# Optimization experiments

Measured on AMD Instinct MI355X. Metric: run time of the kernel, lower is better.

## Reference

```python
import jax, jax.numpy as jnp
import numpy as np

B, N, C = 32, 577, 768
H = 12
DH = C // H  # 64
SCALE = DH ** -0.5


def setup_inputs() -> dict:
    key = jax.random.key(0)
    ks = jax.random.split(key, 5)
    x = jax.random.normal(ks[0], (B, N, C), dtype=jnp.float32)
    # Linear params (torch convention: y = x @ W.T + b)
    qkv_w = jax.random.normal(ks[1], (3 * C, C), dtype=jnp.float32) * (C ** -0.5)
    qkv_b = jnp.zeros((3 * C,), dtype=jnp.float32)
    proj_w = jax.random.normal(ks[2], (C, C), dtype=jnp.float32) * (C ** -0.5)
    proj_b = jnp.zeros((C,), dtype=jnp.float32)
    return {"x": x, "qkv_w": qkv_w, "qkv_b": qkv_b, "proj_w": proj_w, "proj_b": proj_b}


def reference(x, qkv_w, qkv_b, proj_w, proj_b):
    b, n, c = x.shape
    qkv = x @ qkv_w.T + qkv_b                       # [B, N, 3C]
    qkv = qkv.reshape(b, n, 3, H, DH).transpose(2, 0, 3, 1, 4)  # [3, B, H, N, DH]
    q, k, v = qkv[0], qkv[1], qkv[2]
    q = q * SCALE
    attn = jnp.einsum('bhnd,bhmd->bhnm', q, k)      # [B, H, N, N]
    # sigmoid -> inverse-sigmoid straight-through rewrite (forward equals logit(sigmoid(attn)))
    sig = jax.nn.sigmoid(attn)
    inv_sig = jnp.log(sig / (1.0 - sig))
    attn_st = attn + jax.lax.stop_gradient(inv_sig - attn)
    p = jax.nn.softmax(attn_st, axis=-1)
    out = jnp.einsum('bhnm,bhmd->bhnd', p, v)       # [B, H, N, DH]
    out = out.transpose(0, 2, 1, 3).reshape(b, n, c)
    return out @ proj_w.T + proj_b
```

## Files before the change

### kernel.cpp

```cpp
#include <hip/hip_runtime.h>

typedef __bf16 bf16;
typedef __attribute__((ext_vector_type(4))) __bf16 bf16x4;
typedef __attribute__((ext_vector_type(8))) __bf16 bf16x8;
typedef __attribute__((ext_vector_type(4))) float f32x4;

#define MFMA_BF16(A_, B_, C_) __builtin_amdgcn_mfma_f32_16x16x32_bf16(A_, B_, C_, 0, 0, 0)

#define BB    32
#define SEQ   577
#define CH    768
#define NH    12
#define DHD   64
#define MROWS (BB * SEQ)
#define NQKV  2304
#define SEQP  584
#define QSCALE 0.1803368801111204f

__device__ __forceinline__ void async_ld16(const bf16* g, bf16* l) {
  __builtin_amdgcn_global_load_lds(
      (const __attribute__((address_space(1))) void*)g,
      (__attribute__((address_space(3))) void*)l, 16, 0, 0);
}

__global__ __launch_bounds__(256) void cvt_bf16(const float* __restrict__ src,
                                                bf16* __restrict__ dst, int n) {
  int idx = (blockIdx.x * 256 + threadIdx.x) * 4;
  if (idx >= n) return;
  float4 v = *(const float4*)(src + idx);
  bf16x4 o = {(bf16)v.x, (bf16)v.y, (bf16)v.z, (bf16)v.w};
  *(bf16x4*)(dst + idx) = o;
}

template <int EPI>
__global__ __launch_bounds__(256, 5)
void gemm_bt(const bf16* __restrict__ A, const bf16* __restrict__ W,
             const float* __restrict__ bias,
             bf16* __restrict__ qrm, bf16* __restrict__ krm, bf16* __restrict__ vt,
             float* __restrict__ out) {
  __shared__ bf16 As[2][128 * 32];
  __shared__ bf16 Bs[2][128 * 32];
  const int tid = threadIdx.x, lane = tid & 63, wid = tid >> 6;
  const int quad = lane >> 4, r15 = lane & 15;

  const int nbx = (int)gridDim.x;
  const int nwg = nbx * (int)gridDim.y;
  int bid = (int)blockIdx.y * nbx + (int)blockIdx.x;
  int q8 = nwg >> 3, r8 = nwg & 7;
  int xcd = bid & 7, sub = bid >> 3;
  int wg = (xcd < r8 ? xcd * (q8 + 1) : r8 * (q8 + 1) + (xcd - r8) * q8) + sub;
  const int m0 = (wg / nbx) * 128, n0 = (wg % nbx) * 128;
  const int waveM = wid & 1, waveN = wid >> 1;

  const bf16* aSrc[2];
  const bf16* bSrc[2];
  for (int c = 0; c < 2; ++c) {
    int q = wid * 128 + c * 64 + lane;
    int row = q >> 2;
    int sw = (row ^ (row >> 2)) & 3;
    int kc = (q & 3) ^ sw;
    aSrc[c] = A + (size_t)(m0 + row) * CH + kc * 8;
    bSrc[c] = W + (size_t)(n0 + row) * CH + kc * 8;
  }

  f32x4 acc[4][4];
#pragma unroll
  for (int i = 0; i < 4; ++i)
#pragma unroll
    for (int j = 0; j < 4; ++j) acc[i][j] = (f32x4){0.f, 0.f, 0.f, 0.f};

#define GSTAGE(K0, BUF)                                                   \
  {                                                                       \
    _Pragma("unroll") for (int c = 0; c < 2; ++c) {                       \
      async_ld16(aSrc[c] + (K0), &As[BUF][(wid * 128 + c * 64) * 8]);     \
      async_ld16(bSrc[c] + (K0), &Bs[BUF][(wid * 128 + c * 64) * 8]);     \
    }                                                                     \
  }

#define GCOMPUTE(BUF)                                                     \
  {                                                                       \
    bf16x8 af[4], bfr[4];                                                 \
    _Pragma("unroll") for (int s = 0; s < 4; ++s) {                       \
      int rowA = waveM * 64 + s * 16 + r15;                               \
      int ca = quad ^ ((rowA ^ (rowA >> 2)) & 3);                         \
      af[s] = *(const bf16x8*)(&As[BUF][rowA * 32 + ca * 8]);             \
      int rowB = waveN * 64 + s * 16 + r15;                               \
      int cb = quad ^ ((rowB ^ (rowB >> 2)) & 3);                         \
      bfr[s] = *(const bf16x8*)(&Bs[BUF][rowB * 32 + cb * 8]);            \
    }                                                                     \
    _Pragma("unroll") for (int sm = 0; sm < 4; ++sm)                      \
      _Pragma("unroll") for (int sn = 0; sn < 4; ++sn)                    \
        acc[sm][sn] = MFMA_BF16(af[sm], bfr[sn], acc[sm][sn]);            \
  }

  GSTAGE(0, 0);
  for (int k0 = 0; k0 < CH; k0 += 64) {
    __syncthreads();
    GSTAGE(k0 + 32, 1);
    GCOMPUTE(0);
    __syncthreads();
    if (k0 + 64 < CH) GSTAGE(k0 + 64, 0);
    GCOMPUTE(1);
  }

  if (EPI == 0) {
    int t = (n0 >= 1536) ? 2 : (n0 >= 768 ? 1 : 0);
#pragma unroll
    for (int sn = 0; sn < 4; ++sn) {
      int gn = n0 + waveN * 64 + sn * 16 + r15;
      float bv = bias[gn];
      int col = gn - t * CH;
      int h = col >> 6, d = col & 63;
#pragma unroll
      for (int sm = 0; sm < 4; ++sm) {
        int gmBase = m0 + waveM * 64 + sm * 16 + quad * 4;
#pragma unroll
        for (int r = 0; r < 4; ++r) {
          int gm = gmBase + r;
          if (gm < MROWS) {
            float v = acc[sm][sn][r] + bv;
            if (t == 0) {
              qrm[(size_t)gm * CH + col] = (bf16)(v * QSCALE);
            } else if (t == 1) {
              krm[(size_t)gm * CH + col] = (bf16)v;
            } else {
              int b_ = gm / SEQ;
              int n_ = gm - b_ * SEQ;
              vt[((size_t)(b_ * NH + h) * DHD + d) * SEQP + n_] = (bf16)v;
            }
          }
        }
      }
    }
  } else {
#pragma unroll
    for (int sn = 0; sn < 4; ++sn) {
      int gn = n0 + waveN * 64 + sn * 16 + r15;
      float bv = bias[gn];
#pragma unroll
      for (int sm = 0; sm < 4; ++sm) {
        int gmBase = m0 + waveM * 64 + sm * 16 + quad * 4;
#pragma unroll
        for (int r = 0; r < 4; ++r) {
          int gm = gmBase + r;
          if (gm < MROWS) out[(size_t)gm * CH + gn] = acc[sm][sn][r] + bv;
        }
      }
    }
  }
}

__global__ __launch_bounds__(256, 6)
void attn_kernel(const bf16* __restrict__ qrm, const bf16* __restrict__ krm,
                 const bf16* __restrict__ vt, bf16* __restrict__ ob) {
  __shared__ bf16 Ks[64 * 72];
  __shared__ bf16 Vt[64 * 72];
  const int tid = threadIdx.x, lane = tid & 63, wid = tid >> 6;
  const int quad = lane >> 4, r15 = lane & 15;
  const int qt = blockIdx.x, bh = blockIdx.y;
  const int b_ = bh / NH, h = bh - b_ * NH;
  const bf16* vtb = vt + (size_t)bh * DHD * SEQP;

  int qrow = qt * 64 + wid * 16 + r15;
  if (qrow > SEQ - 1) qrow = SEQ - 1;
  const bf16* qp = qrm + (size_t)(b_ * SEQ + qrow) * CH + h * DHD + quad * 8;
  bf16x8 qf0 = *(const bf16x8*)qp;
  bf16x8 qf1 = *(const bf16x8*)(qp + 32);

  f32x4 oacc[4];
#pragma unroll
  for (int i = 0; i < 4; ++i) oacc[i] = (f32x4){0.f, 0.f, 0.f, 0.f};
  float lrow[4] = {0.f, 0.f, 0.f, 0.f};

  for (int j0 = 0; j0 < SEQ; j0 += 64) {
    __syncthreads();
#pragma unroll
    for (int c = 0; c < 2; ++c) {
      int sid = c * 256 + tid;
      int row = sid >> 3, cc = sid & 7;
      int jr = j0 + row;
      if (jr > SEQ - 1) jr = SEQ - 1;
      *(bf16x8*)(Ks + row * 72 + cc * 8) =
          *(const bf16x8*)(krm + (size_t)(b_ * SEQ + jr) * CH + h * DHD + cc * 8);
      int jst = j0 + cc * 8;
      if (jst > SEQ - 1) jst = SEQ - 1;
      *(bf16x8*)(Vt + row * 72 + cc * 8) = *(const bf16x8*)(vtb + (size_t)row * SEQP + jst);
    }
    __syncthreads();

    f32x4 s[4];
#pragma unroll
    for (int sj = 0; sj < 4; ++sj) {
      bf16x8 kf0 = *(const bf16x8*)(Ks + (sj * 16 + r15) * 72 + quad * 8);
      bf16x8 kf1 = *(const bf16x8*)(Ks + (sj * 16 + r15) * 72 + 32 + quad * 8);
      f32x4 z = (f32x4){0.f, 0.f, 0.f, 0.f};
      s[sj] = MFMA_BF16(qf0, kf0, z);
      s[sj] = MFMA_BF16(qf1, kf1, s[sj]);
    }
#pragma unroll
    for (int sj = 0; sj < 4; ++sj)
      if (j0 + sj * 16 + r15 > SEQ - 1) s[sj] = (f32x4){-1e30f, -1e30f, -1e30f, -1e30f};

#pragma unroll
    for (int sj = 0; sj < 4; ++sj)
#pragma unroll
      for (int r = 0; r < 4; ++r) {
        float e = __builtin_amdgcn_exp2f(s[sj][r]);
        s[sj][r] = e;
        lrow[r] += e;
      }

    __syncthreads();
    bf16* Pw = Ks + wid * (16 * 72);
#pragma unroll
    for (int sj = 0; sj < 4; ++sj)
#pragma unroll
      for (int r = 0; r < 4; ++r)
        Pw[(quad * 4 + r) * 72 + sj * 16 + r15] = (bf16)s[sj][r];
    asm volatile("s_waitcnt lgkmcnt(0)" ::: "memory");

#pragma unroll
    for (int kc = 0; kc < 2; ++kc) {
      bf16x8 pf = *(const bf16x8*)(Pw + r15 * 72 + kc * 32 + quad * 8);
#pragma unroll
      for (int sd = 0; sd < 4; ++sd) {
        bf16x8 vf = *(const bf16x8*)(Vt + (sd * 16 + r15) * 72 + kc * 32 + quad * 8);
        oacc[sd] = MFMA_BF16(pf, vf, oacc[sd]);
      }
    }
  }

#pragma unroll
  for (int r = 0; r < 4; ++r) {
    float rs = lrow[r];
    rs += __shfl_xor(rs, 1);
    rs += __shfl_xor(rs, 2);
    rs += __shfl_xor(rs, 4);
    rs += __shfl_xor(rs, 8);
    lrow[r] = rs;
  }

#pragma unroll
  for (int r = 0; r < 4; ++r) {
    int orow = qt * 64 + wid * 16 + quad * 4 + r;
    if (orow < SEQ) {
      float inv = 1.0f / lrow[r];
      size_t rowoff = ((size_t)(b_ * SEQ + orow)) * CH + h * DHD;
#pragma unroll
      for (int sd = 0; sd < 4; ++sd)
        ob[rowoff + sd * 16 + r15] = (bf16)(oacc[sd][r] * inv);
    }
  }
}

extern "C" void kernel_launch(void* const* d_in, const int* in_sizes, int n_in,
                              void* d_out, int out_size, void* d_ws, size_t ws_size,
                              hipStream_t stream) {
  const float* x      = (const float*)d_in[0];
  const float* qkv_w  = (const float*)d_in[1];
  const float* qkv_b  = (const float*)d_in[2];
  const float* proj_w = (const float*)d_in[3];
  const float* proj_b = (const float*)d_in[4];
  float* out = (float*)d_out;

  char* w = (char*)d_ws;
  bf16* xb  = (bf16*)(w);
  bf16* wqp = (bf16*)(w + 28360704);
  bf16* qrm = (bf16*)(w + 31899648);
  bf16* krm = (bf16*)(w + 60260352);
  bf16* vtb = (bf16*)(w + 88621056);

  cvt_bf16<<<(MROWS * CH / 4 + 255) / 256, 256, 0, stream>>>(x, xb, MROWS * CH);
  cvt_bf16<<<(NQKV * CH / 4 + 255) / 256, 256, 0, stream>>>(qkv_w, wqp, NQKV * CH);

  gemm_bt<0><<<dim3(NQKV / 128, 145), 256, 0, stream>>>(
      xb, wqp, qkv_b, qrm, krm, vtb, nullptr);

  attn_kernel<<<dim3(10, BB * NH), 256, 0, stream>>>(qrm, krm, vtb, xb);

  cvt_bf16<<<(CH * CH / 4 + 255) / 256, 256, 0, stream>>>(proj_w, wqp, CH * CH);

  gemm_bt<1><<<dim3(CH / 128, 145), 256, 0, stream>>>(
      xb, wqp, proj_b, nullptr, nullptr, nullptr, out);
}
```

Measured before the change: 410.5 us.

## Split GEMMs into specialized QKV and 256-tile pipelined proj kernels, widen attention tiles

The templated GEMM is split into two kernels. The QKV GEMM drops the XCD remapping and uses launch bounds of 2. The projection GEMM now uses 256x256 tiles with 512 threads and a 4-deep async global-to-LDS pipeline, which raises operand reuse and hides load latency. The attention kernel processes 128 query rows per block, two 16-row groups per wave, so each K/V tile staged in LDS is reused twice, and P gets its own LDS buffer to remove a barrier. A pad_v kernel zeroes the V padding columns. The proj GEMM reads up to row 73*256, past MROWS, which relies on workspace slack beyond the xb buffer.

```diff
diff --git a/kernel.cpp b/kernel.cpp
--- a/kernel.cpp
+++ b/kernel.cpp
@@ -17,6 +17,8 @@
 #define SEQP  584
 #define QSCALE 0.1803368801111204f
 
+#define NSTEP 24
+
 __device__ __forceinline__ void async_ld16(const bf16* g, bf16* l) {
   __builtin_amdgcn_global_load_lds(
       (const __attribute__((address_space(1))) void*)g,
@@ -32,24 +34,24 @@
   *(bf16x4*)(dst + idx) = o;
 }
 
-template <int EPI>
-__global__ __launch_bounds__(256, 5)
-void gemm_bt(const bf16* __restrict__ A, const bf16* __restrict__ W,
-             const float* __restrict__ bias,
-             bf16* __restrict__ qrm, bf16* __restrict__ krm, bf16* __restrict__ vt,
-             float* __restrict__ out) {
+__global__ __launch_bounds__(256) void pad_v(bf16* __restrict__ vt) {
+  int r = blockIdx.x * 256 + threadIdx.x;
+  if (r < BB * NH * DHD) {
+    bf16* p = vt + (size_t)r * SEQP + SEQ;
+#pragma unroll
+    for (int i = 0; i < 7; ++i) p[i] = (bf16)0.f;
+  }
+}
+
+__global__ __launch_bounds__(256, 2)
+void gemm_qkv(const bf16* __restrict__ A, const bf16* __restrict__ W,
+              const float* __restrict__ bias,
+              bf16* __restrict__ qrm, bf16* __restrict__ krm, bf16* __restrict__ vt) {
   __shared__ bf16 As[2][128 * 32];
   __shared__ bf16 Bs[2][128 * 32];
   const int tid = threadIdx.x, lane = tid & 63, wid = tid >> 6;
   const int quad = lane >> 4, r15 = lane & 15;
-
-  const int nbx = (int)gridDim.x;
-  const int nwg = nbx * (int)gridDim.y;
-  int bid = (int)blockIdx.y * nbx + (int)blockIdx.x;
-  int q8 = nwg >> 3, r8 = nwg & 7;
-  int xcd = bid & 7, sub = bid >> 3;
-  int wg = (xcd < r8 ? xcd * (q8 + 1) : r8 * (q8 + 1) + (xcd - r8) * q8) + sub;
-  const int m0 = (wg / nbx) * 128, n0 = (wg % nbx) * 128;
+  const int m0 = blockIdx.y * 128, n0 = blockIdx.x * 128;
   const int waveM = wid & 1, waveN = wid >> 1;
 
   const bf16* aSrc[2];
@@ -103,74 +105,165 @@
     GCOMPUTE(1);
   }
 
-  if (EPI == 0) {
-    int t = (n0 >= 1536) ? 2 : (n0 >= 768 ? 1 : 0);
-#pragma unroll
-    for (int sn = 0; sn < 4; ++sn) {
-      int gn = n0 + waveN * 64 + sn * 16 + r15;
-      float bv = bias[gn];
-      int col = gn - t * CH;
-      int h = col >> 6, d = col & 63;
-#pragma unroll
-      for (int sm = 0; sm < 4; ++sm) {
-        int gmBase = m0 + waveM * 64 + sm * 16 + quad * 4;
-#pragma unroll
-        for (int r = 0; r < 4; ++r) {
-          int gm = gmBase + r;
-          if (gm < MROWS) {
-            float v = acc[sm][sn][r] + bv;
-            if (t == 0) {
-              qrm[(size_t)gm * CH + col] = (bf16)(v * QSCALE);
-            } else if (t == 1) {
-              krm[(size_t)gm * CH + col] = (bf16)v;
-            } else {
-              int b_ = gm / SEQ;
-              int n_ = gm - b_ * SEQ;
-              vt[((size_t)(b_ * NH + h) * DHD + d) * SEQP + n_] = (bf16)v;
-            }
+  int t = (n0 >= 1536) ? 2 : (n0 >= 768 ? 1 : 0);
+#pragma unroll
+  for (int sn = 0; sn < 4; ++sn) {
+    int gn = n0 + waveN * 64 + sn * 16 + r15;
+    float bv = bias[gn];
+    int col = gn - t * CH;
+    int h = col >> 6, d = col & 63;
+#pragma unroll
+    for (int sm = 0; sm < 4; ++sm) {
+      int gmBase = m0 + waveM * 64 + sm * 16 + quad * 4;
+#pragma unroll
+      for (int r = 0; r < 4; ++r) {
+        int gm = gmBase + r;
+        if (gm < MROWS) {
+          float v = acc[sm][sn][r] + bv;
+          if (t == 0) {
+            qrm[(size_t)gm * CH + col] = (bf16)(v * QSCALE);
+          } else if (t == 1) {
+            krm[(size_t)gm * CH + col] = (bf16)v;
+          } else {
+            int b_ = gm / SEQ;
+            int n_ = gm - b_ * SEQ;
+            vt[((size_t)(b_ * NH + h) * DHD + d) * SEQP + n_] = (bf16)v;
           }
         }
       }
     }
-  } else {
-#pragma unroll
-    for (int sn = 0; sn < 4; ++sn) {
-      int gn = n0 + waveN * 64 + sn * 16 + r15;
-      float bv = bias[gn];
-#pragma unroll
-      for (int sm = 0; sm < 4; ++sm) {
-        int gmBase = m0 + waveM * 64 + sm * 16 + quad * 4;
-#pragma unroll
-        for (int r = 0; r < 4; ++r) {
-          int gm = gmBase + r;
-          if (gm < MROWS) out[(size_t)gm * CH + gn] = acc[sm][sn][r] + bv;
-        }
-      }
-    }
-  }
-}
-
-__global__ __launch_bounds__(256, 6)
+  }
+}
+#undef GSTAGE
+#undef GCOMPUTE
+
+__global__ __launch_bounds__(512, 2)
+void gemm_proj(const bf16* __restrict__ A, const bf16* __restrict__ W,
+               const float* __restrict__ bias, float* __restrict__ out) {
+  __shared__ bf16 As[4][256 * 32];
+  __shared__ bf16 Bs[4][256 * 32];
+  const int tid = threadIdx.x, lane = tid & 63, wid = tid >> 6;
+  const int quad = lane >> 4, r15 = lane & 15;
+
+  const int nbx = (int)gridDim.x;
+  const int nwg = nbx * (int)gridDim.y;
+  int bid = (int)blockIdx.y * nbx + (int)blockIdx.x;
+  int q8 = nwg >> 3, r8 = nwg & 7;
+  int xcd = bid & 7, sub = bid >> 3;
+  int wg = (xcd < r8 ? xcd * (q8 + 1) : r8 * (q8 + 1) + (xcd - r8) * q8) + sub;
+  const int m0 = (wg / nbx) * 256, n0 = (wg % nbx) * 256;
+
+  const int rm = (wid >> 2) * 128;
+  const int rn = (wid & 3) * 64;
+
+  int aOff[2], bOff[2];
+#pragma unroll
+  for (int i = 0; i < 2; ++i) {
+    int slot = i * 512 + tid;
+    int row = slot >> 2, pc2 = slot & 3;
+    int gc2 = pc2 ^ ((row ^ (row >> 2)) & 3);
+    aOff[i] = (m0 + row) * CH + gc2 * 8;
+    bOff[i] = (n0 + row) * CH + gc2 * 8;
+  }
+
+  f32x4 acc[8][4];
+#pragma unroll
+  for (int i = 0; i < 8; ++i)
+#pragma unroll
+    for (int j = 0; j < 4; ++j) acc[i][j] = (f32x4){0.f, 0.f, 0.f, 0.f};
+
+#define ISSUE2(S)                                                              \
+  {                                                                            \
+    const int kb_ = (S) * 32;                                                  \
+    const int bf_ = (S) & 3;                                                   \
+    _Pragma("unroll") for (int i = 0; i < 2; ++i) {                            \
+      async_ld16(A + aOff[i] + kb_, &As[bf_][(i * 512 + tid) * 8]);            \
+      async_ld16(W + bOff[i] + kb_, &Bs[bf_][(i * 512 + tid) * 8]);            \
+    }                                                                          \
+  }
+
+#define COMPUTE2(BF)                                                           \
+  {                                                                            \
+    bf16x8 bfr[4], afr[8];                                                     \
+    _Pragma("unroll") for (int sn = 0; sn < 4; ++sn) {                         \
+      int fr = rn + sn * 16 + r15;                                             \
+      int pc2 = quad ^ ((fr ^ (fr >> 2)) & 3);                                 \
+      bfr[sn] = *(const bf16x8*)(&Bs[BF][fr * 32 + pc2 * 8]);                  \
+    }                                                                          \
+    _Pragma("unroll") for (int sm = 0; sm < 8; ++sm) {                         \
+      int fr = rm + sm * 16 + r15;                                             \
+      int pc2 = quad ^ ((fr ^ (fr >> 2)) & 3);                                 \
+      afr[sm] = *(const bf16x8*)(&As[BF][fr * 32 + pc2 * 8]);                  \
+    }                                                                          \
+    _Pragma("unroll") for (int sm = 0; sm < 8; ++sm)                           \
+      _Pragma("unroll") for (int sn = 0; sn < 4; ++sn)                         \
+        acc[sm][sn] = MFMA_BF16(afr[sm], bfr[sn], acc[sm][sn]);                \
+  }
+
+  ISSUE2(0);
+  ISSUE2(1);
+  for (int s = 0; s < NSTEP; ++s) {
+    if (s < NSTEP - 2) {
+      ISSUE2(s + 2);
+      asm volatile("s_waitcnt vmcnt(8)" ::: "memory");
+    } else if (s == NSTEP - 2) {
+      asm volatile("s_waitcnt vmcnt(4)" ::: "memory");
+    } else {
+      asm volatile("s_waitcnt vmcnt(0)" ::: "memory");
+    }
+    __builtin_amdgcn_s_barrier();
+    asm volatile("" ::: "memory");
+    COMPUTE2(s & 3);
+  }
+
+#pragma unroll
+  for (int sn = 0; sn < 4; ++sn) {
+    int gn = n0 + rn + sn * 16 + r15;
+    float bv = bias[gn];
+#pragma unroll
+    for (int sm = 0; sm < 8; ++sm) {
+      int gmBase = m0 + rm + sm * 16 + quad * 4;
+#pragma unroll
+      for (int r = 0; r < 4; ++r) {
+        int gm = gmBase + r;
+        if (gm < MROWS) out[(size_t)gm * CH + gn] = acc[sm][sn][r] + bv;
+      }
+    }
+  }
+}
+#undef ISSUE2
+#undef COMPUTE2
+
+__global__ __launch_bounds__(256, 5)
 void attn_kernel(const bf16* __restrict__ qrm, const bf16* __restrict__ krm,
                  const bf16* __restrict__ vt, bf16* __restrict__ ob) {
   __shared__ bf16 Ks[64 * 72];
   __shared__ bf16 Vt[64 * 72];
+  __shared__ bf16 Ps[4][16 * 72];
   const int tid = threadIdx.x, lane = tid & 63, wid = tid >> 6;
   const int quad = lane >> 4, r15 = lane & 15;
   const int qt = blockIdx.x, bh = blockIdx.y;
   const int b_ = bh / NH, h = bh - b_ * NH;
   const bf16* vtb = vt + (size_t)bh * DHD * SEQP;
 
-  int qrow = qt * 64 + wid * 16 + r15;
-  if (qrow > SEQ - 1) qrow = SEQ - 1;
-  const bf16* qp = qrm + (size_t)(b_ * SEQ + qrow) * CH + h * DHD + quad * 8;
-  bf16x8 qf0 = *(const bf16x8*)qp;
-  bf16x8 qf1 = *(const bf16x8*)(qp + 32);
-
-  f32x4 oacc[4];
-#pragma unroll
-  for (int i = 0; i < 4; ++i) oacc[i] = (f32x4){0.f, 0.f, 0.f, 0.f};
-  float lrow[4] = {0.f, 0.f, 0.f, 0.f};
+  bf16x8 qf[2][2];
+#pragma unroll
+  for (int g = 0; g < 2; ++g) {
+    int qrow = qt * 128 + wid * 32 + g * 16 + r15;
+    if (qrow > SEQ - 1) qrow = SEQ - 1;
+    const bf16* qp = qrm + (size_t)(b_ * SEQ + qrow) * CH + h * DHD + quad * 8;
+    qf[g][0] = *(const bf16x8*)qp;
+    qf[g][1] = *(const bf16x8*)(qp + 32);
+  }
+
+  f32x4 oacc[2][4];
+#pragma unroll
+  for (int g = 0; g < 2; ++g)
+#pragma unroll
+    for (int i = 0; i < 4; ++i) oacc[g][i] = (f32x4){0.f, 0.f, 0.f, 0.f};
+  float lrow[2][4] = {{0.f, 0.f, 0.f, 0.f}, {0.f, 0.f, 0.f, 0.f}};
+
+  bf16* Pw = Ps[wid];
 
   for (int j0 = 0; j0 < SEQ; j0 += 64) {
     __syncthreads();
@@ -188,69 +281,74 @@
     }
     __syncthreads();
 
-    f32x4 s[4];
-#pragma unroll
-    for (int sj = 0; sj < 4; ++sj) {
-      bf16x8 kf0 = *(const bf16x8*)(Ks + (sj * 16 + r15) * 72 + quad * 8);
-      bf16x8 kf1 = *(const bf16x8*)(Ks + (sj * 16 + r15) * 72 + 32 + quad * 8);
-      f32x4 z = (f32x4){0.f, 0.f, 0.f, 0.f};
-      s[sj] = MFMA_BF16(qf0, kf0, z);
-      s[sj] = MFMA_BF16(qf1, kf1, s[sj]);
-    }
-#pragma unroll
-    for (int sj = 0; sj < 4; ++sj)
-      if (j0 + sj * 16 + r15 > SEQ - 1) s[sj] = (f32x4){-1e30f, -1e30f, -1e30f, -1e30f};
-
-#pragma unroll
-    for (int sj = 0; sj < 4; ++sj)
-#pragma unroll
-      for (int r = 0; r < 4; ++r) {
-        float e = __builtin_amdgcn_exp2f(s[sj][r]);
-        s[sj][r] = e;
-        lrow[r] += e;
-      }
-
-    __syncthreads();
-    bf16* Pw = Ks + wid * (16 * 72);
-#pragma unroll
-    for (int sj = 0; sj < 4; ++sj)
-#pragma unroll
-      for (int r = 0; r < 4; ++r)
-        Pw[(quad * 4 + r) * 72 + sj * 16 + r15] = (bf16)s[sj][r];
-    asm volatile("s_waitcnt lgkmcnt(0)" ::: "memory");
-
-#pragma unroll
-    for (int kc = 0; kc < 2; ++kc) {
-      bf16x8 pf = *(const bf16x8*)(Pw + r15 * 72 + kc * 32 + quad * 8);
-#pragma unroll
-      for (int sd = 0; sd < 4; ++sd) {
-        bf16x8 vf = *(const bf16x8*)(Vt + (sd * 16 + r15) * 72 + kc * 32 + quad * 8);
-        oacc[sd] = MFMA_BF16(pf, vf, oacc[sd]);
-      }
-    }
-  }
-
-#pragma unroll
-  for (int r = 0; r < 4; ++r) {
-    float rs = lrow[r];
-    rs += __shfl_xor(rs, 1);
-    rs += __shfl_xor(rs, 2);
-    rs += __shfl_xor(rs, 4);
-    rs += __shfl_xor(rs, 8);
-    lrow[r] = rs;
-  }
-
-#pragma unroll
-  for (int r = 0; r < 4; ++r) {
-    int orow = qt * 64 + wid * 16 + quad * 4 + r;
-    if (orow < SEQ) {
-      float inv = 1.0f / lrow[r];
-      size_t rowoff = ((size_t)(b_ * SEQ + orow)) * CH + h * DHD;
-#pragma unroll
-      for (int sd = 0; sd < 4; ++sd)
-        ob[rowoff + sd * 16 + r15] = (bf16)(oacc[sd][r] * inv);
-    }
-  }
+#pragma unroll
+    for (int g = 0; g < 2; ++g) {
+      f32x4 s[4];
+#pragma unroll
+      for (int sj = 0; sj < 4; ++sj) {
+        bf16x8 kf0 = *(const bf16x8*)(Ks + (sj * 16 + r15) * 72 + quad * 8);
+        bf16x8 kf1 = *(const bf16x8*)(Ks + (sj * 16 + r15) * 72 + 32 + quad * 8);
+        f32x4 z = (f32x4){0.f, 0.f, 0.f, 0.f};
+        s[sj] = MFMA_BF16(qf[g][0], kf0, z);
+        s[sj] = MFMA_BF16(qf[g][1], kf1, s[sj]);
+      }
+#pragma unroll
+      for (int sj = 0; sj < 4; ++sj)
+        if (j0 + sj * 16 + r15 > SEQ - 1) s[sj] = (f32x4){-1e30f, -1e30f, -1e30f, -1e30f};
+
+#pragma unroll
+      for (int sj = 0; sj < 4; ++sj)
+#pragma unroll
+        for (int r = 0; r < 4; ++r) {
+          float e = __builtin_amdgcn_exp2f(s[sj][r]);
+          s[sj][r] = e;
+          lrow[g][r] += e;
+        }
+
+#pragma unroll
+      for (int sj = 0; sj < 4; ++sj)
+#pragma unroll
+        for (int r = 0; r < 4; ++r)
+          Pw[(quad * 4 + r) * 72 + sj * 16 + r15] = (bf16)s[sj][r];
+      asm volatile("s_waitcnt lgkmcnt(0)" ::: "memory");
+
+#pragma unroll
+      for (int kc = 0; kc < 2; ++kc) {
+        bf16x8 pf = *(const bf16x8*)(Pw + r15 * 72 + kc * 32 + quad * 8);
+#pragma unroll
+        for (int sd = 0; sd < 4; ++sd) {
+          bf16x8 vf = *(const bf16x8*)(Vt + (sd * 16 + r15) * 72 + kc * 32 + quad * 8);
+          oacc[g][sd] = MFMA_BF16(pf, vf, oacc[g][sd]);
+        }
+      }
+    }
+  }
+
+#pragma unroll
+  for (int g = 0; g < 2; ++g)
+#pragma unroll
+    for (int r = 0; r < 4; ++r) {
+      float rs = lrow[g][r];
+      rs += __shfl_xor(rs, 1);
+      rs += __shfl_xor(rs, 2);
+      rs += __shfl_xor(rs, 4);
+      rs += __shfl_xor(rs, 8);
+      lrow[g][r] = rs;
+    }
+
+#pragma unroll
+  for (int g = 0; g < 2; ++g)
+#pragma unroll
+    for (int r = 0; r < 4; ++r) {
+      int orow = qt * 128 + wid * 32 + g * 16 + quad * 4 + r;
+      if (orow < SEQ) {
+        float inv = 1.0f / lrow[g][r];
+        size_t rowoff = ((size_t)(b_ * SEQ + orow)) * CH + h * DHD;
+#pragma unroll
+        for (int sd = 0; sd < 4; ++sd)
+          ob[rowoff + sd * 16 + r15] = (bf16)(oacc[g][sd][r] * inv);
+      }
+    }
 }
 
 extern "C" void kernel_launch(void* const* d_in, const int* in_sizes, int n_in,
@@ -272,14 +370,14 @@
 
   cvt_bf16<<<(MROWS * CH / 4 + 255) / 256, 256, 0, stream>>>(x, xb, MROWS * CH);
   cvt_bf16<<<(NQKV * CH / 4 + 255) / 256, 256, 0, stream>>>(qkv_w, wqp, NQKV * CH);
-
-  gemm_bt<0><<<dim3(NQKV / 128, 145), 256, 0, stream>>>(
-      xb, wqp, qkv_b, qrm, krm, vtb, nullptr);
-
-  attn_kernel<<<dim3(10, BB * NH), 256, 0, stream>>>(qrm, krm, vtb, xb);
+  pad_v<<<(BB * NH * DHD + 255) / 256, 256, 0, stream>>>(vtb);
+
+  gemm_qkv<<<dim3(NQKV / 128, 145), 256, 0, stream>>>(
+      xb, wqp, qkv_b, qrm, krm, vtb);
+
+  attn_kernel<<<dim3(5, BB * NH), 256, 0, stream>>>(qrm, krm, vtb, xb);
 
   cvt_bf16<<<(CH * CH / 4 + 255) / 256, 256, 0, stream>>>(proj_w, wqp, CH * CH);
 
-  gemm_bt<1><<<dim3(CH / 128, 145), 256, 0, stream>>>(
-      xb, wqp, proj_b, nullptr, nullptr, nullptr, out);
-}
+  gemm_proj<<<dim3(CH / 256, 73), 512, 0, stream>>>(xb, wqp, proj_b, out);
+}
```

Measured after the change: 376.7 us. 8.2% less time.
